# Optimization experiments

Measured on AMD Instinct MI355X. Metric: run time of the kernel, lower is better.

The kernel has to match this reference:

```python
import jax, jax.numpy as jnp
import numpy as np

DIM = 768
NUM_HEADS = 12
HEAD_DIM = DIM // NUM_HEADS
SCALE = HEAD_DIM ** -0.5
B, N = 8, 1024


def setup_inputs() -> dict:
    key = jax.random.key(0)
    k1, k2, k3, k4, k5 = jax.random.split(key, 5)
    x = jax.random.normal(k1, (B, N, DIM), dtype=jnp.float32)
    # qkv: Linear(dim, 3*dim, bias=False); proj: Linear(dim, dim) with bias
    w_qkv = jax.random.normal(k2, (3 * DIM, DIM), dtype=jnp.float32) * (DIM ** -0.5)
    w_proj = jax.random.normal(k3, (DIM, DIM), dtype=jnp.float32) * (DIM ** -0.5)
    b_proj = jnp.zeros((DIM,), dtype=jnp.float32)
    # learned attention mask parameter, shape (H, L, L) with L >= N
    att_mask = jax.random.normal(k4, (NUM_HEADS, N, N), dtype=jnp.float32)
    return {"x": x, "w_qkv": w_qkv, "w_proj": w_proj, "b_proj": b_proj, "att_mask": att_mask}


def reference(x, w_qkv, w_proj, b_proj, att_mask):
    Bx, Nx, C = x.shape
    # qkv projection -> (3, B, H, N, head_dim)
    qkv = (x @ w_qkv.T).reshape(Bx, Nx, 3, NUM_HEADS, C // NUM_HEADS)
    qkv = jnp.transpose(qkv, (2, 0, 3, 1, 4))
    q, k, v = qkv[0], qkv[1], qkv[2]  # gpd_ratio==active_ratio==1 -> scaling factor 1
    # scores [B, H, N, N]
    attn = jnp.einsum('bhnd,bhmd->bhnm', q, k) * SCALE
    # custom sigmoid mask gating before softmax (broadcast over batch)
    attn = attn * jax.nn.sigmoid(att_mask[:, :Nx, :Nx])[None, :, :, :]
    attn = jax.nn.softmax(attn, axis=-1)
    out = jnp.einsum('bhnm,bhmd->bhnd', attn, v)
    out = jnp.transpose(out, (0, 2, 1, 3)).reshape(Bx, Nx, C)
    return out @ w_proj.T + b_proj
```

## Files before the change

### kernel.cpp

```cpp
#include <hip/hip_runtime.h>
#include <math.h>
#include <stdint.h>

typedef unsigned short u16;
typedef __attribute__((ext_vector_type(8))) short short8;
typedef __attribute__((ext_vector_type(4))) float f32x4;

#define GATE_SCALE 0.18033688011112042f

#if __has_builtin(__builtin_amdgcn_exp2f)
#define FEXP2(x) __builtin_amdgcn_exp2f(x)
#else
#define FEXP2(x) exp2f(x)
#endif

__device__ __forceinline__ u16 f2b(float f) {
    union { float f; unsigned u; } v; v.f = f;
    unsigned r = v.u + 0x7fffu + ((v.u >> 16) & 1u);
    return (u16)(r >> 16);
}
__device__ __forceinline__ u16 f2b_hu(float f) {
    union { float f; unsigned u; } v; v.f = f;
    return (u16)((v.u + 0x8000u) >> 16);
}
__device__ __forceinline__ float b2f(u16 u) {
    union { float f; unsigned u; } v; v.u = ((unsigned)u) << 16; return v.f;
}

#define GLL16(gsrc, ldsbase) __builtin_amdgcn_global_load_lds(                    \
    (__attribute__((address_space(1))) void*)(uintptr_t)(gsrc),                   \
    (__attribute__((address_space(3))) void*)(uint32_t)(uintptr_t)(ldsbase),      \
    16, 0, 0)

#define NX4  1572864
#define NW14 442368
#define NW24 147456
#define NXW4 (NX4 + NW14 + NW24)

__global__ __launch_bounds__(256) void prep_all(
    const float4* __restrict__ x, const float4* __restrict__ wq,
    const float4* __restrict__ wp,
    ushort4* __restrict__ xb, ushort4* __restrict__ wqb,
    ushort4* __restrict__ wpb,
    const float4* __restrict__ mask4, u16* __restrict__ gp)
{
    __shared__ u16 L[64][72];
    const int bx = blockIdx.x;
    const int t = threadIdx.x;

    if (bx >= 3072) {
        size_t i = (size_t)(bx - 3072) * 256 + t;
        float4 v; ushort4* dst; size_t j;
        if (i < NX4)            { j = i;               v = x[j];  dst = xb;  }
        else if (i < NX4 + NW14){ j = i - NX4;         v = wq[j]; dst = wqb; }
        else                    { j = i - (NX4 + NW14);v = wp[j]; dst = wpb; }
        ushort4 o; o.x = f2b(v.x); o.y = f2b(v.y); o.z = f2b(v.z); o.w = f2b(v.w);
        dst[j] = o;
        return;
    }

    const int bid = bx;
    const int kt = bid & 15, qt = (bid >> 4) & 15, h = bid >> 8;

    #pragma unroll
    for (int s = 0; s < 4; ++s) {
        const int idx = t + s * 256;
        const int row = idx >> 4, c4 = idx & 15;
        float4 v = mask4[(size_t)(h * 1024 + qt * 64 + row) * 256 + kt * 16 + c4];
        L[row][c4 * 4 + 0] = f2b(GATE_SCALE / (1.f + __expf(-v.x)));
        L[row][c4 * 4 + 1] = f2b(GATE_SCALE / (1.f + __expf(-v.y)));
        L[row][c4 * 4 + 2] = f2b(GATE_SCALE / (1.f + __expf(-v.z)));
        L[row][c4 * 4 + 3] = f2b(GATE_SCALE / (1.f + __expf(-v.w)));
    }
    __syncthreads();

    const int w = t >> 6, l = t & 63;
    const int fq = l >> 4, fr = l & 15;
    union { u16 u[16]; float4 f[2]; } vals;
    #pragma unroll
    for (int i = 0; i < 4; ++i)
        #pragma unroll
        for (int nt = 0; nt < 4; ++nt)
            vals.u[i * 4 + nt] = L[16 * w + 4 * fq + i][nt * 16 + fr];
    float4* dst = (float4*)(gp + (size_t)bid * 4096 + (size_t)t * 16);
    dst[0] = vals.f[0];
    dst[1] = vals.f[1];
}

__global__ __launch_bounds__(256, 2) void qkv_gemm(
    const u16* __restrict__ xb, const u16* __restrict__ wb,
    u16* __restrict__ qb, u16* __restrict__ kb, u16* __restrict__ vb)
{
    __shared__ u16 As[3][4096];
    __shared__ u16 Bs[3][8192];
    const int t = threadIdx.x, l = t & 63, w = t >> 6;
    const int wc = w * 64;

    const int orig = blockIdx.x;
    const int nid = (orig & 7) * 72 + (orig >> 3);
    const int m0 = (nid / 9) * 128, c0 = (nid % 9) * 256;

    f32x4 acc[8][4];
    #pragma unroll
    for (int i = 0; i < 8; ++i)
        #pragma unroll
        for (int j = 0; j < 4; ++j) { f32x4 z = {0.f,0.f,0.f,0.f}; acc[i][j] = z; }

    const int srow = l >> 2, sseg = l & 3;
    const int gcol = ((sseg ^ ((srow >> 1) & 3)) << 3);
    const u16* aA = xb + (size_t)(m0 + w * 16 + srow) * 768 + gcol;
    const u16* aB = wb + (size_t)(c0 + w * 16 + srow) * 768 + gcol;

    const int fr = l & 15, fq = l >> 4;
    const int fseg = (fq ^ ((fr >> 1) & 3)) << 3;

    auto stage = [&](int bi, int koff) {
        GLL16(aA + koff,                      &As[bi][(w + 0) * 512]);
        GLL16(aA + koff + (size_t)64 * 768,   &As[bi][(w + 4) * 512]);
        GLL16(aB + koff,                      &Bs[bi][(w + 0) * 512]);
        GLL16(aB + koff + (size_t)64 * 768,   &Bs[bi][(w + 4) * 512]);
        GLL16(aB + koff + (size_t)128 * 768,  &Bs[bi][(w + 8) * 512]);
        GLL16(aB + koff + (size_t)192 * 768,  &Bs[bi][(w + 12) * 512]);
    };

    stage(0, 0);
    stage(1, 32);

    int cur = 0;
    for (int kt = 0; kt < 24; ++kt) {
        if (kt < 23) asm volatile("s_waitcnt vmcnt(6)" ::: "memory");
        else         asm volatile("s_waitcnt vmcnt(0)" ::: "memory");
        __builtin_amdgcn_s_barrier();
        if (kt < 22) {
            const int nn = (cur == 0) ? 2 : cur - 1;
            stage(nn, (kt + 2) * 32);
        }
        const u16* A = As[cur];
        const u16* B = Bs[cur];
        short8 af[8], bf[4];
        #pragma unroll
        for (int mt = 0; mt < 8; ++mt)
            af[mt] = *(const short8*)&A[(mt * 16 + fr) * 32 + fseg];
        #pragma unroll
        for (int nt = 0; nt < 4; ++nt)
            bf[nt] = *(const short8*)&B[(wc + nt * 16 + fr) * 32 + fseg];
        #pragma unroll
        for (int mt = 0; mt < 8; ++mt)
            #pragma unroll
            for (int nt = 0; nt < 4; ++nt)
                acc[mt][nt] = __builtin_amdgcn_mfma_f32_16x16x32_bf16(
                    af[mt], bf[nt], acc[mt][nt], 0, 0, 0);
        cur = (cur == 2) ? 0 : cur + 1;
    }

    const int b = m0 >> 10;
    const int n0 = m0 & 1023;
    #pragma unroll
    for (int nt = 0; nt < 4; ++nt) {
        const int c = c0 + wc + nt * 16 + fr;
        const int which = c / 768;
        const int rem = c - which * 768;
        const int h = rem >> 6, d = rem & 63;
        if (which < 2) {
            u16* dst = ((which == 0) ? qb : kb)
                       + ((size_t)(b * 12 + h) * 1024) * 64 + d;
            #pragma unroll
            for (int mt = 0; mt < 8; ++mt)
                #pragma unroll
                for (int r = 0; r < 4; ++r) {
                    const int n = n0 + mt * 16 + fq * 4 + r;
                    dst[(size_t)n * 64] = f2b(acc[mt][nt][r]);
                }
        } else {
            u16* dst = vb + ((size_t)(b * 12 + h) * 64 + d) * 1024
                          + n0 + fq * 4;
            #pragma unroll
            for (int mt = 0; mt < 8; ++mt) {
                ushort4 pk;
                pk.x = f2b(acc[mt][nt][0]); pk.y = f2b(acc[mt][nt][1]);
                pk.z = f2b(acc[mt][nt][2]); pk.w = f2b(acc[mt][nt][3]);
                *(ushort4*)(dst + mt * 16) = pk;
            }
        }
    }
}

__global__ __launch_bounds__(256, 3) void flash_attn(
    const u16* __restrict__ qb, const u16* __restrict__ kb,
    const u16* __restrict__ vt, const u16* __restrict__ gperm,
    u16* __restrict__ aob)
{
    __shared__ u16 Ks[2][4096], Vts[2][4096], Ps[4096];
    const int t = threadIdx.x, l = t & 63, w = t >> 6;
    const int bid = blockIdx.x;
    const int xcd = bid & 7, jj = bid >> 3;
    const int bh = (jj % 12) * 8 + xcd;
    const int qtb = jj / 12;
    const int h = bh % 12, b = bh / 12;
    const int q0 = qtb * 128;

    const u16* hq = qb + (size_t)bh * 65536;
    const u16* hk = kb + (size_t)bh * 65536;
    const u16* hv = vt + (size_t)bh * 65536;
    const u16* hgb = gperm + ((size_t)h * 256 + qtb * 32) * 4096 + (w * 64 + l) * 16;

    const int sr = l >> 3, ss = l & 7;
    const int sg = ((ss ^ (sr & 7)) << 3);
    const int j0 = w * 2, j1 = j0 + 1;

    const int fq = l >> 4, fr = l & 15;
    const int sega = ((fq ^ (fr & 7)) << 3);
    const int segb = (((4 + fq) ^ (fr & 7)) << 3);

    short8 aq[2][2];
    #pragma unroll
    for (int qh = 0; qh < 2; ++qh) {
        const u16* qrow = hq + (size_t)(q0 + qh * 64 + 16 * w + fr) * 64;
        aq[qh][0] = *(const short8*)(qrow + fq * 8);
        aq[qh][1] = *(const short8*)(qrow + 32 + fq * 8);
    }

    GLL16(hk + (size_t)(j0 * 8 + sr) * 64 + sg, &Ks[0][j0 * 512]);
    GLL16(hk + (size_t)(j1 * 8 + sr) * 64 + sg, &Ks[0][j1 * 512]);
    GLL16(hv + (size_t)(j0 * 8 + sr) * 1024 + sg, &Vts[0][j0 * 512]);
    GLL16(hv + (size_t)(j1 * 8 + sr) * 1024 + sg, &Vts[0][j1 * 512]);
    __builtin_amdgcn_sched_barrier(0);

    short8 gn[4];
    gn[0] = *(const short8*)(hgb);
    gn[1] = *(const short8*)(hgb + 8);
    gn[2] = *(const short8*)(hgb + 65536);
    gn[3] = *(const short8*)(hgb + 65536 + 8);

    float l_part[2][4] = {{0.f,0.f,0.f,0.f},{0.f,0.f,0.f,0.f}};
    f32x4 o[2][4];
    #pragma unroll
    for (int qh = 0; qh < 2; ++qh)
        #pragma unroll
        for (int nt = 0; nt < 4; ++nt) { f32x4 z = {0.f,0.f,0.f,0.f}; o[qh][nt] = z; }

    for (int kt = 0; kt < 16; ++kt) {
        asm volatile("s_waitcnt vmcnt(4)" ::: "memory");
        __builtin_amdgcn_s_barrier();

        if (kt < 15) {
            const size_t ko = (size_t)(kt + 1) * 64;
            u16* kd = &Ks[(kt + 1) & 1][0];
            u16* vd = &Vts[(kt + 1) & 1][0];
            GLL16(hk + (ko + j0 * 8 + sr) * 64 + sg, kd + j0 * 512);
            GLL16(hk + (ko + j1 * 8 + sr) * 64 + sg, kd + j1 * 512);
            GLL16(hv + (size_t)(j0 * 8 + sr) * 1024 + ko + sg, vd + j0 * 512);
            GLL16(hv + (size_t)(j1 * 8 + sr) * 1024 + ko + sg, vd + j1 * 512);
            __builtin_amdgcn_sched_barrier(0);
        }

        short8 g[4];
        #pragma unroll
        for (int s = 0; s < 4; ++s) g[s] = gn[s];
        if (kt < 15) {
            const size_t go = (size_t)(kt + 1) * 4096;
            gn[0] = *(const short8*)(hgb + go);
            gn[1] = *(const short8*)(hgb + go + 8);
            gn[2] = *(const short8*)(hgb + 65536 + go);
            gn[3] = *(const short8*)(hgb + 65536 + go + 8);
        }

        const u16* KS = &Ks[kt & 1][0];
        const u16* VS = &Vts[kt & 1][0];

        f32x4 sv[2][4];
        __builtin_amdgcn_s_setprio(1);
        #pragma unroll
        for (int nt = 0; nt < 4; ++nt) {
            short8 kf0 = *(const short8*)&KS[(nt * 16 + fr) * 64 + sega];
            short8 kf1 = *(const short8*)&KS[(nt * 16 + fr) * 64 + segb];
            f32x4 z0 = {0.f,0.f,0.f,0.f};
            z0 = __builtin_amdgcn_mfma_f32_16x16x32_bf16(aq[0][0], kf0, z0, 0, 0, 0);
            z0 = __builtin_amdgcn_mfma_f32_16x16x32_bf16(aq[0][1], kf1, z0, 0, 0, 0);
            sv[0][nt] = z0;
            f32x4 z1 = {0.f,0.f,0.f,0.f};
            z1 = __builtin_amdgcn_mfma_f32_16x16x32_bf16(aq[1][0], kf0, z1, 0, 0, 0);
            z1 = __builtin_amdgcn_mfma_f32_16x16x32_bf16(aq[1][1], kf1, z1, 0, 0, 0);
            sv[1][nt] = z1;
        }
        __builtin_amdgcn_s_setprio(0);

        short8 ap[2][2];
        #pragma unroll
        for (int qh = 0; qh < 2; ++qh) {
            #pragma unroll
            for (int i = 0; i < 4; ++i) {
                const int pr = 4 * fq + i;
                #pragma unroll
                for (int nt = 0; nt < 4; ++nt) {
                    const int idx = i * 4 + nt;
                    const float gv = b2f((u16)(idx < 8 ? g[2 * qh][idx]
                                                       : g[2 * qh + 1][idx - 8]));
                    const float p = FEXP2(sv[qh][nt][i] * gv);
                    l_part[qh][i] += p;
                    const int col = nt * 16 + fr;
                    Ps[w * 1024 + pr * 64 + (((col >> 3) ^ (pr & 7)) << 3) + (col & 7)]
                        = f2b_hu(p);
                }
            }
            ap[qh][0] = *(const short8*)&Ps[w * 1024 + fr * 64 + sega];
            ap[qh][1] = *(const short8*)&Ps[w * 1024 + fr * 64 + segb];
        }

        __builtin_amdgcn_s_setprio(1);
        #pragma unroll
        for (int nt = 0; nt < 4; ++nt) {
            short8 vf0 = *(const short8*)&VS[(nt * 16 + fr) * 64 + sega];
            short8 vf1 = *(const short8*)&VS[(nt * 16 + fr) * 64 + segb];
            o[0][nt] = __builtin_amdgcn_mfma_f32_16x16x32_bf16(ap[0][0], vf0, o[0][nt], 0, 0, 0);
            o[0][nt] = __builtin_amdgcn_mfma_f32_16x16x32_bf16(ap[0][1], vf1, o[0][nt], 0, 0, 0);
            o[1][nt] = __builtin_amdgcn_mfma_f32_16x16x32_bf16(ap[1][0], vf0, o[1][nt], 0, 0, 0);
            o[1][nt] = __builtin_amdgcn_mfma_f32_16x16x32_bf16(ap[1][1], vf1, o[1][nt], 0, 0, 0);
        }
        __builtin_amdgcn_s_setprio(0);
    }

    #pragma unroll
    for (int qh = 0; qh < 2; ++qh) {
        #pragma unroll
        for (int i = 0; i < 4; ++i) {
            float s = l_part[qh][i];
            s += __shfl_xor(s, 1, 16);
            s += __shfl_xor(s, 2, 16);
            s += __shfl_xor(s, 4, 16);
            s += __shfl_xor(s, 8, 16);
            const float inv = 1.f / s;
            const int n = q0 + qh * 64 + 16 * w + 4 * fq + i;
            const size_t rowoff = ((size_t)b * 1024 + n) * 768 + h * 64;
            #pragma unroll
            for (int nt = 0; nt < 4; ++nt)
                aob[rowoff + nt * 16 + fr] = f2b(o[qh][nt][i] * inv);
        }
    }
}

__global__ __launch_bounds__(256, 2) void proj_gemm(
    const u16* __restrict__ aob, const u16* __restrict__ wb,
    const float* __restrict__ bproj, float* __restrict__ out)
{
    __shared__ u16 As[3][4096];
    __shared__ u16 Bs[3][8192];
    const int t = threadIdx.x, l = t & 63, w = t >> 6;
    const int wc = w * 64;

    const int orig = blockIdx.x;
    const int nid = (orig & 7) * 24 + (orig >> 3);
    const int m0 = (nid / 3) * 128, c0 = (nid % 3) * 256;

    f32x4 acc[8][4];
    #pragma unroll
    for (int i = 0; i < 8; ++i)
        #pragma unroll
        for (int j = 0; j < 4; ++j) { f32x4 z = {0.f,0.f,0.f,0.f}; acc[i][j] = z; }

    const int srow = l >> 2, sseg = l & 3;
    const int gcol = ((sseg ^ ((srow >> 1) & 3)) << 3);
    const u16* aA = aob + (size_t)(m0 + w * 16 + srow) * 768 + gcol;
    const u16* aB = wb + (size_t)(c0 + w * 16 + srow) * 768 + gcol;

    const int fr = l & 15, fq = l >> 4;
    const int fseg = (fq ^ ((fr >> 1) & 3)) << 3;

    auto stage = [&](int bi, int koff) {
        GLL16(aA + koff,                      &As[bi][(w + 0) * 512]);
        GLL16(aA + koff + (size_t)64 * 768,   &As[bi][(w + 4) * 512]);
        GLL16(aB + koff,                      &Bs[bi][(w + 0) * 512]);
        GLL16(aB + koff + (size_t)64 * 768,   &Bs[bi][(w + 4) * 512]);
        GLL16(aB + koff + (size_t)128 * 768,  &Bs[bi][(w + 8) * 512]);
        GLL16(aB + koff + (size_t)192 * 768,  &Bs[bi][(w + 12) * 512]);
    };

    stage(0, 0);
    stage(1, 32);

    int cur = 0;
    for (int kt = 0; kt < 24; ++kt) {
        if (kt < 23) asm volatile("s_waitcnt vmcnt(6)" ::: "memory");
        else         asm volatile("s_waitcnt vmcnt(0)" ::: "memory");
        __builtin_amdgcn_s_barrier();
        if (kt < 22) {
            const int nn = (cur == 0) ? 2 : cur - 1;
            stage(nn, (kt + 2) * 32);
        }
        const u16* A = As[cur];
        const u16* B = Bs[cur];
        short8 af[8], bf[4];
        #pragma unroll
        for (int mt = 0; mt < 8; ++mt)
            af[mt] = *(const short8*)&A[(mt * 16 + fr) * 32 + fseg];
        #pragma unroll
        for (int nt = 0; nt < 4; ++nt)
            bf[nt] = *(const short8*)&B[(wc + nt * 16 + fr) * 32 + fseg];
        #pragma unroll
        for (int mt = 0; mt < 8; ++mt)
            #pragma unroll
            for (int nt = 0; nt < 4; ++nt)
                acc[mt][nt] = __builtin_amdgcn_mfma_f32_16x16x32_bf16(
                    af[mt], bf[nt], acc[mt][nt], 0, 0, 0);
        cur = (cur == 2) ? 0 : cur + 1;
    }

    #pragma unroll
    for (int nt = 0; nt < 4; ++nt) {
        const int c = c0 + wc + nt * 16 + fr;
        const float bias = bproj[c];
        #pragma unroll
        for (int mt = 0; mt < 8; ++mt)
            #pragma unroll
            for (int r = 0; r < 4; ++r) {
                const int m = m0 + mt * 16 + fq * 4 + r;
                out[(size_t)m * 768 + c] = acc[mt][nt][r] + bias;
            }
    }
}

extern "C" void kernel_launch(void* const* d_in, const int* in_sizes, int n_in,
                              void* d_out, int out_size, void* d_ws, size_t ws_size,
                              hipStream_t stream)
{
    const float* x     = (const float*)d_in[0];
    const float* wqkv  = (const float*)d_in[1];
    const float* wproj = (const float*)d_in[2];
    const float* bproj = (const float*)d_in[3];
    const float* mask  = (const float*)d_in[4];
    float* out = (float*)d_out;

    char* ws = (char*)d_ws;
    u16* gperm  = (u16*)(ws);
    u16* xb     = (u16*)(ws + 25165824);
    u16* wqkvb  = (u16*)(ws + 37748736);
    u16* wprojb = (u16*)(ws + 41287680);
    u16* qb     = (u16*)(ws + 42467328);
    u16* kb     = (u16*)(ws + 55050240);
    u16* vb     = (u16*)(ws + 67633152);
    u16* aob    = (u16*)(ws + 80216064);

    prep_all<<<3072 + NXW4 / 256, 256, 0, stream>>>(
        (const float4*)x, (const float4*)wqkv, (const float4*)wproj,
        (ushort4*)xb, (ushort4*)wqkvb, (ushort4*)wprojb,
        (const float4*)mask, gperm);

    qkv_gemm<<<576, 256, 0, stream>>>(xb, wqkvb, qb, kb, vb);

    flash_attn<<<768, 256, 0, stream>>>(qb, kb, vb, gperm, aob);

    proj_gemm<<<192, 256, 0, stream>>>(aob, wprojb, bproj, out);
}
```

Baseline: 226.8 us.

## Transpose QK^T MFMA output so each lane owns a query row, packing P stores

Swaps the MFMA operands for S = QK^T so the accumulator holds a transposed tile in which each lane owns one query row and four key columns. The precomputed gate layout is permuted to match. Softmax numerators are now packed with v_cvt_pk_bf16_f32 into 8-byte LDS stores using a new swizzle, replacing sixteen scalar bf16 stores. Row sums accumulate per lane, so the per-row 16-lane shuffle reductions collapse into two cross-quad shuffles plus a broadcast at the end. This aims to cut VALU and LDS store instruction count in the softmax stage, at the cost of layout and swizzle correctness risk.

```diff
diff --git a/kernel.cpp b/kernel.cpp
--- a/kernel.cpp
+++ b/kernel.cpp
@@ -81,7 +81,7 @@
     for (int i = 0; i < 4; ++i)
         #pragma unroll
         for (int nt = 0; nt < 4; ++nt)
-            vals.u[i * 4 + nt] = L[16 * w + 4 * fq + i][nt * 16 + fr];
+            vals.u[i * 4 + nt] = L[16 * w + fr][nt * 16 + 4 * fq + i];
     float4* dst = (float4*)(gp + (size_t)bid * 4096 + (size_t)t * 16);
     dst[0] = vals.f[0];
     dst[1] = vals.f[1];
@@ -232,7 +232,7 @@
     gn[2] = *(const short8*)(hgb + 65536);
     gn[3] = *(const short8*)(hgb + 65536 + 8);
 
-    float l_part[2][4] = {{0.f,0.f,0.f,0.f},{0.f,0.f,0.f,0.f}};
+    float l_sum[2] = {0.f, 0.f};
     f32x4 o[2][4];
     #pragma unroll
     for (int qh = 0; qh < 2; ++qh)
@@ -275,12 +275,12 @@
             short8 kf0 = *(const short8*)&KS[(nt * 16 + fr) * 64 + sega];
             short8 kf1 = *(const short8*)&KS[(nt * 16 + fr) * 64 + segb];
             f32x4 z0 = {0.f,0.f,0.f,0.f};
-            z0 = __builtin_amdgcn_mfma_f32_16x16x32_bf16(aq[0][0], kf0, z0, 0, 0, 0);
-            z0 = __builtin_amdgcn_mfma_f32_16x16x32_bf16(aq[0][1], kf1, z0, 0, 0, 0);
+            z0 = __builtin_amdgcn_mfma_f32_16x16x32_bf16(kf0, aq[0][0], z0, 0, 0, 0);
+            z0 = __builtin_amdgcn_mfma_f32_16x16x32_bf16(kf1, aq[0][1], z0, 0, 0, 0);
             sv[0][nt] = z0;
             f32x4 z1 = {0.f,0.f,0.f,0.f};
-            z1 = __builtin_amdgcn_mfma_f32_16x16x32_bf16(aq[1][0], kf0, z1, 0, 0, 0);
-            z1 = __builtin_amdgcn_mfma_f32_16x16x32_bf16(aq[1][1], kf1, z1, 0, 0, 0);
+            z1 = __builtin_amdgcn_mfma_f32_16x16x32_bf16(kf0, aq[1][0], z1, 0, 0, 0);
+            z1 = __builtin_amdgcn_mfma_f32_16x16x32_bf16(kf1, aq[1][1], z1, 0, 0, 0);
             sv[1][nt] = z1;
         }
         __builtin_amdgcn_s_setprio(0);
@@ -289,19 +289,22 @@
         #pragma unroll
         for (int qh = 0; qh < 2; ++qh) {
             #pragma unroll
-            for (int i = 0; i < 4; ++i) {
-                const int pr = 4 * fq + i;
-                #pragma unroll
-                for (int nt = 0; nt < 4; ++nt) {
-                    const int idx = i * 4 + nt;
-                    const float gv = b2f((u16)(idx < 8 ? g[2 * qh][idx]
-                                                       : g[2 * qh + 1][idx - 8]));
-                    const float p = FEXP2(sv[qh][nt][i] * gv);
-                    l_part[qh][i] += p;
-                    const int col = nt * 16 + fr;
-                    Ps[w * 1024 + pr * 64 + (((col >> 3) ^ (pr & 7)) << 3) + (col & 7)]
-                        = f2b_hu(p);
-                }
+            for (int nt = 0; nt < 4; ++nt) {
+                const float g0 = b2f((u16)g[2 * qh][nt]);
+                const float g1 = b2f((u16)g[2 * qh][4 + nt]);
+                const float g2 = b2f((u16)g[2 * qh + 1][nt]);
+                const float g3 = b2f((u16)g[2 * qh + 1][4 + nt]);
+                const float p0 = FEXP2(sv[qh][nt][0] * g0);
+                const float p1 = FEXP2(sv[qh][nt][1] * g1);
+                const float p2 = FEXP2(sv[qh][nt][2] * g2);
+                const float p3 = FEXP2(sv[qh][nt][3] * g3);
+                l_sum[qh] += (p0 + p1) + (p2 + p3);
+                unsigned lo, hi;
+                asm("v_cvt_pk_bf16_f32 %0, %1, %2" : "=v"(lo) : "v"(p0), "v"(p1));
+                asm("v_cvt_pk_bf16_f32 %0, %1, %2" : "=v"(hi) : "v"(p2), "v"(p3));
+                uint2 pk2; pk2.x = lo; pk2.y = hi;
+                *(uint2*)&Ps[w * 1024 + fr * 64
+                             + 4 * ((4 * nt + fq) ^ (2 * (fr & 7)))] = pk2;
             }
             ap[qh][0] = *(const short8*)&Ps[w * 1024 + fr * 64 + sega];
             ap[qh][1] = *(const short8*)&Ps[w * 1024 + fr * 64 + segb];
@@ -322,14 +325,12 @@
 
     #pragma unroll
     for (int qh = 0; qh < 2; ++qh) {
+        float s = l_sum[qh];
+        s += __shfl_xor(s, 16, 64);
+        s += __shfl_xor(s, 32, 64);
         #pragma unroll
         for (int i = 0; i < 4; ++i) {
-            float s = l_part[qh][i];
-            s += __shfl_xor(s, 1, 16);
-            s += __shfl_xor(s, 2, 16);
-            s += __shfl_xor(s, 4, 16);
-            s += __shfl_xor(s, 8, 16);
-            const float inv = 1.f / s;
+            const float inv = 1.f / __shfl(s, (fq << 4) | (4 * fq + i), 64);
             const int n = q0 + qh * 64 + 16 * w + 4 * fq + i;
             const size_t rowoff = ((size_t)b * 1024 + n) * 768 + h * 64;
             #pragma unroll
```

After: 231.5 us. 1.02x slower.

## Shrink QKV GEMM tile to 128x128 with 2x2 warp grid and double buffering

Applied to the files above, without the earlier changes.

The QKV projection GEMM moves from 128x256 tiles (4 warps each covering all 128 rows and 64 columns, triple-buffered LDS) to 128x128 tiles with a 2x2 warp layout and double-buffered LDS. The grid doubles to 1152 blocks, and the XCD-aware block remapping is adjusted to match. Smaller tiles and less LDS per block raise occupancy and parallelism across CUs. The cost is lower arithmetic intensity and a shallower prefetch pipeline: the loop now waits for vmcnt(0) each iteration, so it can overlap loads with MFMA less.

```diff
diff --git a/kernel.cpp b/kernel.cpp
--- a/kernel.cpp
+++ b/kernel.cpp
@@ -87,77 +87,71 @@
     dst[1] = vals.f[1];
 }
 
-__global__ __launch_bounds__(256, 2) void qkv_gemm(
+__global__ __launch_bounds__(256) void qkv_gemm(
     const u16* __restrict__ xb, const u16* __restrict__ wb,
     u16* __restrict__ qb, u16* __restrict__ kb, u16* __restrict__ vb)
 {
-    __shared__ u16 As[3][4096];
-    __shared__ u16 Bs[3][8192];
+    __shared__ u16 As[2][4096];
+    __shared__ u16 Bs[2][4096];
     const int t = threadIdx.x, l = t & 63, w = t >> 6;
-    const int wc = w * 64;
-
-    const int orig = blockIdx.x;
-    const int nid = (orig & 7) * 72 + (orig >> 3);
-    const int m0 = (nid / 9) * 128, c0 = (nid % 9) * 256;
-
-    f32x4 acc[8][4];
-    #pragma unroll
-    for (int i = 0; i < 8; ++i)
+    const int wm = (w & 1) * 64, wn = (w >> 1) * 64;
+
+    const int orig = blockIdx.x + 18 * blockIdx.y;
+    const int nid = (orig & 7) * 144 + (orig >> 3);
+    const int m0 = (nid / 18) * 128, c0 = (nid % 18) * 128;
+
+    f32x4 acc[4][4];
+    #pragma unroll
+    for (int i = 0; i < 4; ++i)
         #pragma unroll
         for (int j = 0; j < 4; ++j) { f32x4 z = {0.f,0.f,0.f,0.f}; acc[i][j] = z; }
 
     const int srow = l >> 2, sseg = l & 3;
     const int gcol = ((sseg ^ ((srow >> 1) & 3)) << 3);
-    const u16* aA = xb + (size_t)(m0 + w * 16 + srow) * 768 + gcol;
-    const u16* aB = wb + (size_t)(c0 + w * 16 + srow) * 768 + gcol;
+    const u16* a0 = xb + (size_t)(m0 + w * 16 + srow) * 768 + gcol;
+    const u16* a1 = a0 + (size_t)64 * 768;
+    const u16* b0p = wb + (size_t)(c0 + w * 16 + srow) * 768 + gcol;
+    const u16* b1p = b0p + (size_t)64 * 768;
+    const int wofs = w * 512;
 
     const int fr = l & 15, fq = l >> 4;
     const int fseg = (fq ^ ((fr >> 1) & 3)) << 3;
 
     auto stage = [&](int bi, int koff) {
-        GLL16(aA + koff,                      &As[bi][(w + 0) * 512]);
-        GLL16(aA + koff + (size_t)64 * 768,   &As[bi][(w + 4) * 512]);
-        GLL16(aB + koff,                      &Bs[bi][(w + 0) * 512]);
-        GLL16(aB + koff + (size_t)64 * 768,   &Bs[bi][(w + 4) * 512]);
-        GLL16(aB + koff + (size_t)128 * 768,  &Bs[bi][(w + 8) * 512]);
-        GLL16(aB + koff + (size_t)192 * 768,  &Bs[bi][(w + 12) * 512]);
+        GLL16(a0 + koff, &As[bi][wofs]);
+        GLL16(a1 + koff, &As[bi][2048 + wofs]);
+        GLL16(b0p + koff, &Bs[bi][wofs]);
+        GLL16(b1p + koff, &Bs[bi][2048 + wofs]);
     };
 
     stage(0, 0);
-    stage(1, 32);
-
-    int cur = 0;
+
     for (int kt = 0; kt < 24; ++kt) {
-        if (kt < 23) asm volatile("s_waitcnt vmcnt(6)" ::: "memory");
-        else         asm volatile("s_waitcnt vmcnt(0)" ::: "memory");
+        asm volatile("s_waitcnt vmcnt(0)" ::: "memory");
         __builtin_amdgcn_s_barrier();
-        if (kt < 22) {
-            const int nn = (cur == 0) ? 2 : cur - 1;
-            stage(nn, (kt + 2) * 32);
-        }
-        const u16* A = As[cur];
-        const u16* B = Bs[cur];
-        short8 af[8], bf[4];
-        #pragma unroll
-        for (int mt = 0; mt < 8; ++mt)
-            af[mt] = *(const short8*)&A[(mt * 16 + fr) * 32 + fseg];
+        if (kt < 23) stage((kt + 1) & 1, (kt + 1) * 32);
+        const u16* A = As[kt & 1];
+        const u16* B = Bs[kt & 1];
+        short8 af[4], bf[4];
+        #pragma unroll
+        for (int mt = 0; mt < 4; ++mt)
+            af[mt] = *(const short8*)&A[(wm + mt * 16 + fr) * 32 + fseg];
         #pragma unroll
         for (int nt = 0; nt < 4; ++nt)
-            bf[nt] = *(const short8*)&B[(wc + nt * 16 + fr) * 32 + fseg];
-        #pragma unroll
-        for (int mt = 0; mt < 8; ++mt)
+            bf[nt] = *(const short8*)&B[(wn + nt * 16 + fr) * 32 + fseg];
+        #pragma unroll
+        for (int mt = 0; mt < 4; ++mt)
             #pragma unroll
             for (int nt = 0; nt < 4; ++nt)
                 acc[mt][nt] = __builtin_amdgcn_mfma_f32_16x16x32_bf16(
                     af[mt], bf[nt], acc[mt][nt], 0, 0, 0);
-        cur = (cur == 2) ? 0 : cur + 1;
     }
 
     const int b = m0 >> 10;
     const int n0 = m0 & 1023;
     #pragma unroll
     for (int nt = 0; nt < 4; ++nt) {
-        const int c = c0 + wc + nt * 16 + fr;
+        const int c = c0 + wn + nt * 16 + fr;
         const int which = c / 768;
         const int rem = c - which * 768;
         const int h = rem >> 6, d = rem & 63;
@@ -165,17 +159,17 @@
             u16* dst = ((which == 0) ? qb : kb)
                        + ((size_t)(b * 12 + h) * 1024) * 64 + d;
             #pragma unroll
-            for (int mt = 0; mt < 8; ++mt)
+            for (int mt = 0; mt < 4; ++mt)
                 #pragma unroll
                 for (int r = 0; r < 4; ++r) {
-                    const int n = n0 + mt * 16 + fq * 4 + r;
+                    const int n = n0 + wm + mt * 16 + fq * 4 + r;
                     dst[(size_t)n * 64] = f2b(acc[mt][nt][r]);
                 }
         } else {
             u16* dst = vb + ((size_t)(b * 12 + h) * 64 + d) * 1024
-                          + n0 + fq * 4;
-            #pragma unroll
-            for (int mt = 0; mt < 8; ++mt) {
+                          + n0 + wm + fq * 4;
+            #pragma unroll
+            for (int mt = 0; mt < 4; ++mt) {
                 ushort4 pk;
                 pk.x = f2b(acc[mt][nt][0]); pk.y = f2b(acc[mt][nt][1]);
                 pk.z = f2b(acc[mt][nt][2]); pk.w = f2b(acc[mt][nt][3]);
@@ -445,7 +439,7 @@
         (ushort4*)xb, (ushort4*)wqkvb, (ushort4*)wprojb,
         (const float4*)mask, gperm);
 
-    qkv_gemm<<<576, 256, 0, stream>>>(xb, wqkvb, qb, kb, vb);
+    qkv_gemm<<<dim3(18, 64), 256, 0, stream>>>(xb, wqkvb, qb, kb, vb);
 
     flash_attn<<<768, 256, 0, stream>>>(qb, kb, vb, gperm, aob);
 
```

Result: no change. 230.7 us (+1.7%).
